# Performance work log

Hardware: AMD Instinct MI355X
Metric: run time of the kernel (lower is better)

The kernel has to match this reference:

```python
import math
import jax, jax.numpy as jnp
import numpy as np

H = 16          # num attention heads
D = 64          # head dim
BUCKETS = 256   # position_buckets
MAX_POS = 512   # max_relative_positions
ATT_SPAN = BUCKETS  # pos_ebd_size A
SCALE_FACTOR = 3    # 1 + len(['c2p','p2c'])


def _log_bucket(rel):
    # log-bucketed relative positions (DeBERTa-v2 _make_log_bucket_position)
    mid = BUCKETS // 2
    rel = jnp.clip(rel, -MAX_POS + 1, MAX_POS - 1)
    sign = jnp.sign(rel).astype(jnp.float32)
    abs_pos = jnp.maximum(jnp.abs(rel), 1)
    log_base = math.log((MAX_POS - 1) / mid)
    log_pos = jnp.ceil(jnp.log(abs_pos.astype(jnp.float32) / mid) / log_base * (mid - 1)) + mid
    bucket = jnp.where(abs_pos < mid, abs_pos.astype(jnp.float32), log_pos) * sign
    return bucket.astype(jnp.int32)


def _rel_pos(q_len, k_len):
    q = jnp.arange(q_len, dtype=jnp.int32)
    k = jnp.arange(k_len, dtype=jnp.int32)
    return _log_bucket(q[:, None] - k[None, :])  # (Q, K)


def setup_inputs() -> dict:
    key = jax.random.key(0)
    ks = jax.random.split(key, 6)
    B, S, Hd = 4, 1024, 1024
    std = 0.02
    return {
        "hidden_states": jax.random.normal(ks[0], (B, S, Hd), jnp.float32),
        "rel_embeddings": jax.random.normal(ks[1], (2 * ATT_SPAN, Hd), jnp.float32) * std,
        "Wq": jax.random.normal(ks[2], (Hd, H * D), jnp.float32) * std,
        "bq": jnp.zeros((H * D,), jnp.float32),
        "Wk": jax.random.normal(ks[3], (Hd, H * D), jnp.float32) * std,
        "bk": jnp.zeros((H * D,), jnp.float32),
        "Wv": jax.random.normal(ks[4], (Hd, H * D), jnp.float32) * std,
        "bv": jnp.zeros((H * D,), jnp.float32),
    }


def reference(hidden_states, rel_embeddings, Wq, bq, Wk, bk, Wv, bv):
    B, S, Hd = hidden_states.shape
    A2 = 2 * ATT_SPAN

    def heads(x):  # (B,S,H*D) -> (B,H,S,D)
        return x.reshape(B, S, H, D).transpose(0, 2, 1, 3)

    q = heads(hidden_states @ Wq + bq)
    k = heads(hidden_states @ Wk + bk)
    v = heads(hidden_states @ Wv + bv)

    scale = math.sqrt(D * SCALE_FACTOR)
    scores = jnp.einsum('bhqd,bhkd->bhqk', q, k) / scale  # (B,H,S,S)

    rel = _rel_pos(S, S)  # (S,S) int32 bucketed relative ids
    # share_att_key=True: pos key/query use key_proj/query_proj
    pos_k = (rel_embeddings @ Wk + bk).reshape(A2, H, D).transpose(1, 0, 2)  # (H,2A,D)
    pos_q = (rel_embeddings @ Wq + bq).reshape(A2, H, D).transpose(1, 0, 2)  # (H,2A,D)

    # c2p: content->position
    c2p = jnp.einsum('bhqd,hkd->bhqk', q, pos_k)  # (B,H,S,2A)
    c2p_idx = jnp.clip(rel + ATT_SPAN, 0, A2 - 1)  # (S,S)
    c2p = jnp.take_along_axis(c2p, jnp.broadcast_to(c2p_idx[None, None], (B, H, S, S)), axis=-1) / scale

    # p2c: position->content
    p2c = jnp.einsum('bhkd,hqd->bhkq', k, pos_q)  # (B,H,S,2A)
    p2c_idx = jnp.clip(-rel + ATT_SPAN, 0, A2 - 1)  # (S,S)
    p2c = jnp.take_along_axis(p2c, jnp.broadcast_to(p2c_idx[None, None], (B, H, S, S)), axis=-1)
    p2c = jnp.swapaxes(p2c, -1, -2) / scale

    probs = jax.nn.softmax(scores + c2p + p2c, axis=-1)
    ctx = jnp.einsum('bhqk,bhkd->bhqd', probs, v)  # (B,H,S,D)
    return ctx.transpose(0, 2, 1, 3).reshape(B, S, H * D)
```

## Files before the change

### kernel.cpp

```cpp
#include <hip/hip_runtime.h>
#include <hip/hip_bf16.h>
#include <math.h>

typedef __attribute__((ext_vector_type(8))) short v8s;
typedef __attribute__((ext_vector_type(4))) short v4sh;
typedef __attribute__((ext_vector_type(4))) unsigned short v4us;
typedef __attribute__((ext_vector_type(4))) float v4f;
typedef __attribute__((ext_vector_type(4))) int   v4i;

#define AS1(p) ((const __attribute__((address_space(1))) void*)(p))
#define AS3(p) ((__attribute__((address_space(3))) void*)(p))

__device__ inline unsigned short f2b(float f){
  __hip_bfloat16 h = __float2bfloat16(f);
  return __builtin_bit_cast(unsigned short, h);
}
__device__ inline float b2f(unsigned short u){
  __hip_bfloat16 h = __builtin_bit_cast(__hip_bfloat16, u);
  return __bfloat162float(h);
}
__device__ inline unsigned cvtpk(float lo, float hi){
  unsigned d;
  asm("v_cvt_pk_bf16_f32 %0, %1, %2" : "=v"(d) : "v"(lo), "v"(hi));
  return d;
}

__device__ inline int bucket_id(int i){
  int r = i - 1023;
  if (r > 511) r = 511; if (r < -511) r = -511;
  float sign = (r > 0) ? 1.f : ((r < 0) ? -1.f : 0.f);
  int ap = r < 0 ? -r : r; if (ap < 1) ap = 1;
  float bucket;
  if (ap < 128) bucket = (float)ap * sign;
  else {
    float lp = ceilf(logf((float)ap / 128.f) / logf(511.f/128.f) * 127.f) + 128.f;
    bucket = lp * sign;
  }
  int idx = (int)bucket + 256;
  if (idx < 0) idx = 0; if (idx > 511) idx = 511;
  return idx;
}

__global__ __launch_bounds__(256) void pack_x(const float* __restrict__ hs,
                                              const float* __restrict__ rel,
                                              const float* __restrict__ Wq,
                                              const float* __restrict__ Wk,
                                              const float* __restrict__ Wv,
                                              unsigned short* __restrict__ X,
                                              unsigned short* __restrict__ Wt3,
                                              short* __restrict__ tab,
                                              unsigned long long* __restrict__ tab64){
  __shared__ unsigned short t[64][65];
  int blk = blockIdx.x;
  if (blk < 2304){
    const int HT8 = 4096*1024/8;
    int i8 = blk*256 + threadIdx.x;
    const float* src = (i8 < HT8) ? (hs + (size_t)i8*8) : (rel + ((size_t)i8 - HT8)*8);
    v8s o;
    #pragma unroll
    for (int j = 0; j < 8; j++) o[j] = (short)f2b(src[j]);
    *(v8s*)&X[(size_t)i8*8] = o;
    return;
  }
  if (blk < 2313){
    int i = (blk - 2304)*256 + threadIdx.x;
    if (i < 2047) tab[i] = (short)bucket_id(i);
    if (i < 2056){
      unsigned long long w = 0;
      #pragma unroll
      for (int r = 0; r < 4; r++)
        w |= (unsigned long long)(unsigned short)bucket_id(i + r) << (16*r);
      tab64[i] = w;
    }
    return;
  }
  int tb = blk - 2313;
  int wsel = tb >> 8, bx = tb & 255;
  const float* in = (wsel == 0) ? Wq : ((wsel == 1) ? Wk : Wv);
  unsigned short* outp = Wt3 + ((size_t)wsel << 20);
  int r0 = (bx >> 4) << 6, c0 = (bx & 15) << 6;
  int tx = threadIdx.x & 63, ty = threadIdx.x >> 6;
  #pragma unroll
  for (int p = 0; p < 16; p++){ int r = (p<<2)+ty; t[tx][r] = f2b(in[(size_t)(r0+r)*1024 + c0+tx]); }
  __syncthreads();
  #pragma unroll
  for (int p = 0; p < 16; p++){ int c = (p<<2)+ty; outp[(size_t)(c0+c)*1024 + r0+tx] = t[c][tx]; }
}

__global__ __launch_bounds__(256) void gemm_qkv(
    const unsigned short* __restrict__ A,
    const unsigned short* __restrict__ Bt3,
    unsigned short* __restrict__ Qa, unsigned short* __restrict__ Ka,
    unsigned short* __restrict__ VtT,
    const float* __restrict__ bq, const float* __restrict__ bk,
    const float* __restrict__ bv, float alpha_q)
{
  __shared__ unsigned short smem[2*128*64];
  unsigned short* a_tile = smem;
  unsigned short* b_tile = smem + 128*64;
  int nb = (blockIdx.x & 7)*108 + (blockIdx.x >> 3);
  int bm = nb / 24, bn = nb % 24;
  int m0 = bm << 7, n0 = bn << 7;
  int tid = threadIdx.x, lane = tid & 63, wave = tid >> 6;
  int l15 = lane & 15, lhi = lane >> 4;
  int rbase = (wave >> 1) << 6, cbase = (wave & 1) << 6;
  int crow[4], csw[4];
  #pragma unroll
  for (int u = 0; u < 4; u++){
    int ch = tid + (u << 8);
    crow[u] = ch >> 3;
    csw[u] = ((ch & 7) ^ (crow[u] & 7)) << 3;
  }
  v4f acc[4][4] = {};
  for (int kt = 0; kt < 1024; kt += 64){
    #pragma unroll
    for (int u = 0; u < 4; u++){
      int ch = tid + (u << 8);
      __builtin_amdgcn_global_load_lds(AS1(A   + (size_t)(m0 + crow[u])*1024 + kt + csw[u]),
                                       AS3(a_tile + (size_t)ch*8), 16, 0, 0);
      __builtin_amdgcn_global_load_lds(AS1(Bt3 + (size_t)(n0 + crow[u])*1024 + kt + csw[u]),
                                       AS3(b_tile + (size_t)ch*8), 16, 0, 0);
    }
    __syncthreads();
    #pragma unroll
    for (int ks = 0; ks < 2; ks++){
      v8s af[4], bfr[4];
      int kb = (ks << 2) + lhi;
      #pragma unroll
      for (int i = 0; i < 4; i++){
        int r = rbase + (i << 4) + l15;
        af[i] = *(const v8s*)&a_tile[r*64 + ((kb ^ (r & 7)) << 3)];
      }
      #pragma unroll
      for (int j = 0; j < 4; j++){
        int r = cbase + (j << 4) + l15;
        bfr[j] = *(const v8s*)&b_tile[r*64 + ((kb ^ (r & 7)) << 3)];
      }
      #pragma unroll
      for (int i = 0; i < 4; i++)
        #pragma unroll
        for (int j = 0; j < 4; j++)
          acc[i][j] = __builtin_amdgcn_mfma_f32_16x16x32_bf16(af[i], bfr[j], acc[i][j], 0, 0, 0);
    }
    __syncthreads();
  }
  int seg = n0 >> 10;
  int nn0 = n0 & 1023;
  if (seg == 2){
    if (m0 >= 4096) return;
    int bb = m0 >> 10, s0 = m0 & 1023;
    #pragma unroll
    for (int i = 0; i < 4; i++){
      int r = rbase + (i << 4) + (lhi << 2);
      #pragma unroll
      for (int j = 0; j < 4; j++){
        int c = cbase + (j << 4) + l15;
        float bvv = bv[nn0 + c];
        #pragma unroll
        for (int rr = 0; rr < 4; rr++)
          smem[c*128 + ((r + rr) ^ ((c & 7) << 4))] = f2b(acc[i][j][rr] + bvv);
      }
    }
    __syncthreads();
    int v = tid >> 3, sc = (tid & 7) << 4;
    #pragma unroll
    for (int vb = 0; vb < 4; vb++){
      int vv = v + (vb << 5);
      #pragma unroll
      for (int c2 = 0; c2 < 2; c2++){
        int sb = sc + (c2 << 3);
        v8s val = *(const v8s*)&smem[vv*128 + (sb ^ ((vv & 7) << 4))];
        *(v8s*)&VtT[((size_t)(bb << 10) + nn0 + vv)*1024 + s0 + sb] = val;
      }
    }
    return;
  }
  unsigned short* C = (seg == 0) ? Qa : Ka;
  const float* bias = (seg == 0) ? bq : bk;
  float alpha = (seg == 0) ? alpha_q : 1.f;
  #pragma unroll
  for (int i = 0; i < 4; i++){
    int row = m0 + rbase + (i << 4) + (lhi << 2);
    #pragma unroll
    for (int j = 0; j < 4; j++){
      int col = nn0 + cbase + (j << 4) + l15;
      float bvv = bias[col];
      #pragma unroll
      for (int r = 0; r < 4; r++)
        C[(size_t)(row + r)*1024 + col] = f2b((acc[i][j][r] + bvv) * alpha);
    }
  }
}

__global__ __launch_bounds__(256) void gemm_pos(
    const unsigned short* __restrict__ Qa,
    const unsigned short* __restrict__ Ka,
    unsigned short* __restrict__ C2P,
    unsigned short* __restrict__ P2C)
{
  __shared__ unsigned short a_tile[128*64];
  __shared__ unsigned short b_tile[128*64];
  int tab = blockIdx.y >> 4, h = blockIdx.y & 15;
  int bm = blockIdx.x >> 2, bn = blockIdx.x & 3;
  int m0 = bm << 7, n0 = bn << 7;
  const unsigned short* A  = tab ? Ka : Qa;
  const unsigned short* Bt = tab ? Qa : Ka;
  unsigned short* C = tab ? P2C : C2P;
  int tid = threadIdx.x, lane = tid & 63, wave = tid >> 6;
  int l15 = lane & 15, lhi = lane >> 4;
  int rbase = (wave >> 1) << 6, cbase = (wave & 1) << 6;
  #pragma unroll
  for (int u = 0; u < 4; u++){
    int ch = tid + (u << 8);
    int row = ch >> 3;
    int csw = ((ch & 7) ^ (row & 7)) << 3;
    __builtin_amdgcn_global_load_lds(AS1(A  + (size_t)(m0 + row)*1024 + (h << 6) + csw),
                                     AS3(a_tile + (size_t)ch*8), 16, 0, 0);
    __builtin_amdgcn_global_load_lds(AS1(Bt + (size_t)(4096 + n0 + row)*1024 + (h << 6) + csw),
                                     AS3(b_tile + (size_t)ch*8), 16, 0, 0);
  }
  __syncthreads();
  v4f acc[4][4] = {};
  #pragma unroll
  for (int ks = 0; ks < 2; ks++){
    v8s af[4], bfr[4];
    int kb = (ks << 2) + lhi;
    #pragma unroll
    for (int i = 0; i < 4; i++){
      int r = rbase + (i << 4) + l15;
      af[i] = *(const v8s*)&a_tile[r*64 + ((kb ^ (r & 7)) << 3)];
    }
    #pragma unroll
    for (int j = 0; j < 4; j++){
      int r = cbase + (j << 4) + l15;
      bfr[j] = *(const v8s*)&b_tile[r*64 + ((kb ^ (r & 7)) << 3)];
    }
    #pragma unroll
    for (int i = 0; i < 4; i++)
      #pragma unroll
      for (int j = 0; j < 4; j++)
        acc[i][j] = __builtin_amdgcn_mfma_f32_16x16x32_bf16(af[i], bfr[j], acc[i][j], 0, 0, 0);
  }
  #pragma unroll
  for (int i = 0; i < 4; i++){
    int row = m0 + rbase + (i << 4) + (lhi << 2);
    #pragma unroll
    for (int j = 0; j < 4; j++){
      int col = n0 + cbase + (j << 4) + l15;
      #pragma unroll
      for (int r = 0; r < 4; r++)
        C[(size_t)(row + r)*8192 + (h << 9) + col] = f2b(acc[i][j][r]);
    }
  }
}

__global__ __launch_bounds__(256) void attn(
  const unsigned short* __restrict__ Qall,
  const unsigned short* __restrict__ Kall,
  const unsigned short* __restrict__ Vt,
  const unsigned short* __restrict__ c2p,
  const unsigned short* __restrict__ p2c,
  const short* __restrict__ idxt,
  const unsigned long long* __restrict__ t64g,
  float* __restrict__ out)
{
  __shared__ unsigned short k_lds[64*64];
  __shared__ unsigned short v_lds[2][64*64];
  __shared__ unsigned short cw[64*72];
  __shared__ unsigned short pw[64*72];
  __shared__ short basc[16*64];
  __shared__ short basp[16*64];

  int bid = blockIdx.x;
  int xcd = bid & 7, jj = bid >> 3;
  int bh = (xcd << 3) + (jj >> 4), qb = jj & 15;
  int b = bh >> 4, h = bh & 15;
  int q0 = qb << 6;
  int tid = threadIdx.x, lane = tid & 63, wave = tid >> 6;
  int l15 = lane & 15, lhi = lane >> 4;

  #pragma unroll
  for (int v = 0; v < 8; v++){
    int i = tid + (v << 8);
    int kt = (i >> 6) & 15, row = i & 63;
    if (i < 1024){
      int bc = idxt[q0 + row - (kt << 6) + 960] & ~7;
      basc[(kt << 6) + row] = (short)(row*72 - bc);
    } else {
      int bp = idxt[q0 + 1023 - (kt << 6) - row] & ~7;
      basp[(kt << 6) + row] = (short)(row*72 - bp);
    }
  }

  int qrow = q0 + (wave << 4) + l15;
  v8s aq[2];
  #pragma unroll
  for (int ks = 0; ks < 2; ks++)
    aq[ks] = *(const v8s*)&Qall[(size_t)((b << 10) + qrow)*1024 + (h << 6) + (ks << 5) + (lhi << 3)];

  int prow_[3], pcc_[3]; bool pval[3];
  #pragma unroll
  for (int u = 0; u < 3; u++){
    int pp = tid + (u << 8);
    pval[u] = pp < 576;
    prow_[u] = pp / 9; pcc_[u] = pp - prow_[u]*9;
  }
  const size_t cbase0 = ((size_t)((b << 10) + q0))*8192 + (h << 9);
  const size_t pbase0 = ((size_t)(b << 10))*8192 + (h << 9);

  unsigned long long t64u[4];

  auto issue_kwin = [&](int kt){
    int k0 = kt << 6;
    #pragma unroll
    for (int u = 0; u < 2; u++){
      int ch = tid + (u << 8);
      int rr = ch >> 3, seg = ch & 7;
      int csw = (seg ^ (rr & 7)) << 3;
      __builtin_amdgcn_global_load_lds(AS1(Kall + (size_t)((b << 10) + k0 + rr)*1024 + (h << 6) + csw),
                                       AS3(k_lds + (size_t)ch*8), 16, 0, 0);
    }
    #pragma unroll
    for (int u = 0; u < 3; u++){
      if (pval[u]){
        int row = prow_[u], cc = pcc_[u];
        int bc = row*72 - (int)basc[(kt << 6) + row];
        __builtin_amdgcn_global_load_lds(AS1(c2p + cbase0 + (size_t)row*8192 + bc + (cc << 3)),
                                         AS3(cw + (size_t)(tid + (u << 8))*8), 16, 0, 0);
        int bp = row*72 - (int)basp[(kt << 6) + row];
        __builtin_amdgcn_global_load_lds(AS1(p2c + pbase0 + (size_t)(k0 + row)*8192 + bp + (cc << 3)),
                                         AS3(pw + (size_t)(tid + (u << 8))*8), 16, 0, 0);
      }
    }
  };
  auto issue_tv = [&](int kt, int sel){
    int k0 = kt << 6;
    int Bc = q0 - k0 + (wave << 4) + l15 - (lhi << 2) + 1020;
    #pragma unroll
    for (int j = 0; j < 4; j++) t64u[j] = t64g[Bc - (j << 4)];
    __builtin_amdgcn_sched_barrier(0);
    #pragma unroll
    for (int u = 0; u < 2; u++){
      int ch = tid + (u << 8);
      int rr = ch >> 3, seg = ch & 7;
      int csw = (seg ^ (rr & 7)) << 3;
      __builtin_amdgcn_global_load_lds(AS1(Vt + (size_t)((b << 10) + (h << 6) + rr)*1024 + k0 + csw),
                                       AS3(&v_lds[sel][0] + (size_t)ch*8), 16, 0, 0);
    }
  };

  v4f o_acc[4] = {};
  float m_run = -INFINITY, l_part = 0.f;

  __syncthreads();
  issue_kwin(0);
  __builtin_amdgcn_sched_barrier(0);
  issue_tv(0, 0);

  for (int kt = 0; kt < 16; kt++){
    asm volatile("s_waitcnt vmcnt(6)" ::: "memory");
    __builtin_amdgcn_sched_barrier(0);
    __builtin_amdgcn_s_barrier();
    __builtin_amdgcn_sched_barrier(0);

    v4f s_acc[4] = {};
    #pragma unroll
    for (int j = 0; j < 4; j++){
      int krow = (j << 4) + l15;
      #pragma unroll
      for (int ks = 0; ks < 2; ks++){
        v8s kf = *(const v8s*)&k_lds[krow*64 + ((((ks << 2) + lhi) ^ (krow & 7)) << 3)];
        s_acc[j] = __builtin_amdgcn_mfma_f32_16x16x32_bf16(kf, aq[ks], s_acc[j], 0, 0, 0);
      }
    }
    int cvq = (int)basc[(kt << 6) + (wave << 4) + l15];
    #pragma unroll
    for (int j = 0; j < 4; j++){
      v4sh bp4 = *(const v4sh*)&basp[(kt << 6) + (j << 4) + (lhi << 2)];
      v4us idv = __builtin_bit_cast(v4us, t64u[j]);
      #pragma unroll
      for (int r = 0; r < 4; r++){
        int id = (int)idv[3 - r];
        s_acc[j][r] += b2f(cw[cvq + id]) + b2f(pw[(int)bp4[r] + id]);
      }
    }
    float lmax = s_acc[0][0];
    #pragma unroll
    for (int j = 0; j < 4; j++)
      #pragma unroll
      for (int r = 0; r < 4; r++) lmax = fmaxf(lmax, s_acc[j][r]);
    if (__any(lmax > m_run + 6.f)){
      float mx = lmax;
      mx = fmaxf(mx, __shfl_xor(mx, 16));
      mx = fmaxf(mx, __shfl_xor(mx, 32));
      float mnew = fmaxf(m_run, mx);
      float corr = exp2f(m_run - mnew);
      m_run = mnew;
      l_part *= corr;
      float co[4];
      #pragma unroll
      for (int r = 0; r < 4; r++) co[r] = __shfl(corr, (lhi << 2) + r);
      #pragma unroll
      for (int j = 0; j < 4; j++)
        #pragma unroll
        for (int r = 0; r < 4; r++) o_acc[j][r] *= co[r];
    }
    unsigned wj[4][2];
    float ps = 0.f;
    #pragma unroll
    for (int j = 0; j < 4; j++){
      float p0 = exp2f(s_acc[j][0] - m_run);
      float p1 = exp2f(s_acc[j][1] - m_run);
      float p2 = exp2f(s_acc[j][2] - m_run);
      float p3 = exp2f(s_acc[j][3] - m_run);
      ps += (p0 + p1) + (p2 + p3);
      wj[j][0] = cvtpk(p0, p1);
      wj[j][1] = cvtpk(p2, p3);
    }
    l_part += ps;
    #pragma unroll
    for (int p = 0; p < 2; p++){
      asm("v_permlane32_swap_b32 %0, %1" : "+v"(wj[0][p]), "+v"(wj[1][p]));
      asm("v_permlane32_swap_b32 %0, %1" : "+v"(wj[2][p]), "+v"(wj[3][p]));
      asm("v_permlane16_swap_b32 %0, %1" : "+v"(wj[0][p]), "+v"(wj[1][p]));
      asm("v_permlane16_swap_b32 %0, %1" : "+v"(wj[2][p]), "+v"(wj[3][p]));
    }
    v4i pai0 = { (int)wj[0][0], (int)wj[0][1], (int)wj[1][0], (int)wj[1][1] };
    v4i pai1 = { (int)wj[2][0], (int)wj[2][1], (int)wj[3][0], (int)wj[3][1] };
    v8s pa0 = __builtin_bit_cast(v8s, pai0);
    v8s pa1 = __builtin_bit_cast(v8s, pai1);

    asm volatile("s_waitcnt vmcnt(0)" ::: "memory");
    __builtin_amdgcn_sched_barrier(0);
    __builtin_amdgcn_s_barrier();
    __builtin_amdgcn_sched_barrier(0);

    if (kt < 15) issue_kwin(kt + 1);
    __builtin_amdgcn_sched_barrier(0);

    const unsigned short* vl = &v_lds[kt & 1][0];
    #pragma unroll
    for (int j = 0; j < 4; j++){
      int vrow = (j << 4) + l15;
      v8s vb0 = *(const v8s*)&vl[vrow*64 + (((lhi) ^ (vrow & 7)) << 3)];
      o_acc[j] = __builtin_amdgcn_mfma_f32_16x16x32_bf16(pa0, vb0, o_acc[j], 0, 0, 0);
      v8s vb1 = *(const v8s*)&vl[vrow*64 + (((4 + lhi) ^ (vrow & 7)) << 3)];
      o_acc[j] = __builtin_amdgcn_mfma_f32_16x16x32_bf16(pa1, vb1, o_acc[j], 0, 0, 0);
    }
    __builtin_amdgcn_sched_barrier(0);
    if (kt < 15) issue_tv(kt + 1, (kt + 1) & 1);
  }
  float ls = l_part;
  ls += __shfl_xor(ls, 16);
  ls += __shfl_xor(ls, 32);
  float inv = 1.f / ls;
  float io[4];
  #pragma unroll
  for (int r = 0; r < 4; r++) io[r] = __shfl(inv, (lhi << 2) + r);
  #pragma unroll
  for (int r = 0; r < 4; r++){
    int row = q0 + (wave << 4) + (lhi << 2) + r;
    #pragma unroll
    for (int j = 0; j < 4; j++)
      out[(size_t)((b << 10) + row)*1024 + (h << 6) + (j << 4) + l15] = o_acc[j][r] * io[r];
  }
}

extern "C" void kernel_launch(void* const* d_in, const int* in_sizes, int n_in,
                              void* d_out, int out_size, void* d_ws, size_t ws_size,
                              hipStream_t stream)
{
  const float* hs  = (const float*)d_in[0];
  const float* rel = (const float*)d_in[1];
  const float* Wq  = (const float*)d_in[2];
  const float* bq  = (const float*)d_in[3];
  const float* Wk  = (const float*)d_in[4];
  const float* bk  = (const float*)d_in[5];
  const float* Wv  = (const float*)d_in[6];
  const float* bv  = (const float*)d_in[7];
  float* out = (float*)d_out;

  char* ws = (char*)d_ws;
  size_t off = 0;
  auto alloc = [&](size_t bytes) -> void* {
    void* p = ws + off; off += (bytes + 255) & ~(size_t)255; return p;
  };
  short*              idxt  = (short*)             alloc(2047 * 2);
  unsigned long long* tab64 = (unsigned long long*)alloc(2056 * 8);
  unsigned short* Xb   = (unsigned short*)alloc((size_t)4608*1024*2);
  unsigned short* Wt3  = (unsigned short*)alloc((size_t)3072*1024*2);
  unsigned short* Qa   = (unsigned short*)alloc((size_t)4608*1024*2);
  unsigned short* Ka   = (unsigned short*)alloc((size_t)4608*1024*2);
  unsigned short* VtT  = (unsigned short*)alloc((size_t)4096*1024*2);
  unsigned short* C2P  = (unsigned short*)alloc((size_t)4096*8192*2);
  unsigned short* P2C  = (unsigned short*)alloc((size_t)4096*8192*2);
  (void)                                  alloc(4096);
  (void)ws_size; (void)in_sizes; (void)n_in; (void)out_size;

  pack_x<<<3081, 256, 0, stream>>>(hs, rel, Wq, Wk, Wv, Xb, Wt3, idxt, tab64);

  const float alpha_q = 1.4426950408889634f / sqrtf(192.f);
  gemm_qkv<<<864, 256, 0, stream>>>(Xb, Wt3, Qa, Ka, VtT, bq, bk, bv, alpha_q);

  gemm_pos<<<dim3(128, 32), 256, 0, stream>>>(Qa, Ka, C2P, P2C);

  attn<<<1024, 256, 0, stream>>>(Qa, Ka, VtT, C2P, P2C, idxt, tab64, out);
}
```

Baseline: 167.6 us.

## Stage GEMM epilogues through LDS for coalesced stores; single-buffer V tile

The projection and positional GEMM epilogues now write bf16 results into a swizzled LDS tile, then store them with coalesced 16-byte vector writes instead of scattered 2-byte global stores. In the attention kernel the double-buffered V tile becomes a single buffer, with an extra barrier before the next V prefetch. This cuts LDS use, which may raise occupancy, at the cost of an added sync per iteration and less overlap between the PV matmul and the next V load.

```diff
diff --git a/kernel.cpp b/kernel.cpp
--- a/kernel.cpp
+++ b/kernel.cpp
@@ -180,15 +180,23 @@
   float alpha = (seg == 0) ? alpha_q : 1.f;
   #pragma unroll
   for (int i = 0; i < 4; i++){
-    int row = m0 + rbase + (i << 4) + (lhi << 2);
-    #pragma unroll
-    for (int j = 0; j < 4; j++){
-      int col = nn0 + cbase + (j << 4) + l15;
-      float bvv = bias[col];
+    int row = rbase + (i << 4) + (lhi << 2);
+    #pragma unroll
+    for (int j = 0; j < 4; j++){
+      int col = cbase + (j << 4) + l15;
+      float bvv = bias[nn0 + col];
       #pragma unroll
       for (int r = 0; r < 4; r++)
-        C[(size_t)(row + r)*1024 + col] = f2b((acc[i][j][r] + bvv) * alpha);
-    }
+        smem[(row + r)*128 + (col ^ (((row + r) & 7) << 4))] = f2b((acc[i][j][r] + bvv) * alpha);
+    }
+  }
+  __syncthreads();
+  #pragma unroll
+  for (int c = 0; c < 8; c++){
+    int row = (tid >> 4) + (c << 4);
+    int col8 = (tid & 15) << 3;
+    v8s val = *(const v8s*)&smem[row*128 + (col8 ^ ((row & 7) << 4))];
+    *(v8s*)&C[(size_t)(m0 + row)*1024 + nn0 + col8] = val;
   }
 }
 
@@ -198,8 +206,9 @@
     unsigned short* __restrict__ C2P,
     unsigned short* __restrict__ P2C)
 {
-  __shared__ unsigned short a_tile[128*64];
-  __shared__ unsigned short b_tile[128*64];
+  __shared__ unsigned short smem[2*128*64];
+  unsigned short* a_tile = smem;
+  unsigned short* b_tile = smem + 128*64;
   int tab = blockIdx.y >> 4, h = blockIdx.y & 15;
   int bm = blockIdx.x >> 2, bn = blockIdx.x & 3;
   int m0 = bm << 7, n0 = bn << 7;
@@ -241,16 +250,25 @@
       for (int j = 0; j < 4; j++)
         acc[i][j] = __builtin_amdgcn_mfma_f32_16x16x32_bf16(af[i], bfr[j], acc[i][j], 0, 0, 0);
   }
+  __syncthreads();
   #pragma unroll
   for (int i = 0; i < 4; i++){
-    int row = m0 + rbase + (i << 4) + (lhi << 2);
-    #pragma unroll
-    for (int j = 0; j < 4; j++){
-      int col = n0 + cbase + (j << 4) + l15;
+    int row = rbase + (i << 4) + (lhi << 2);
+    #pragma unroll
+    for (int j = 0; j < 4; j++){
+      int col = cbase + (j << 4) + l15;
       #pragma unroll
       for (int r = 0; r < 4; r++)
-        C[(size_t)(row + r)*8192 + (h << 9) + col] = f2b(acc[i][j][r]);
-    }
+        smem[(row + r)*128 + (col ^ (((row + r) & 7) << 4))] = f2b(acc[i][j][r]);
+    }
+  }
+  __syncthreads();
+  #pragma unroll
+  for (int c = 0; c < 8; c++){
+    int row = (tid >> 4) + (c << 4);
+    int col8 = (tid & 15) << 3;
+    v8s val = *(const v8s*)&smem[row*128 + (col8 ^ ((row & 7) << 4))];
+    *(v8s*)&C[(size_t)(m0 + row)*8192 + (h << 9) + n0 + col8] = val;
   }
 }
 
@@ -265,7 +283,7 @@
   float* __restrict__ out)
 {
   __shared__ unsigned short k_lds[64*64];
-  __shared__ unsigned short v_lds[2][64*64];
+  __shared__ unsigned short v_lds[64*64];
   __shared__ unsigned short cw[64*72];
   __shared__ unsigned short pw[64*72];
   __shared__ short basc[16*64];
@@ -327,13 +345,13 @@
         int bc = row*72 - (int)basc[(kt << 6) + row];
         __builtin_amdgcn_global_load_lds(AS1(c2p + cbase0 + (size_t)row*8192 + bc + (cc << 3)),
                                          AS3(cw + (size_t)(tid + (u << 8))*8), 16, 0, 0);
-        int bp = row*72 - (int)basp[(kt << 6) + row];
+      int bp = row*72 - (int)basp[(kt << 6) + row];
         __builtin_amdgcn_global_load_lds(AS1(p2c + pbase0 + (size_t)(k0 + row)*8192 + bp + (cc << 3)),
                                          AS3(pw + (size_t)(tid + (u << 8))*8), 16, 0, 0);
       }
     }
   };
-  auto issue_tv = [&](int kt, int sel){
+  auto issue_tv = [&](int kt){
     int k0 = kt << 6;
     int Bc = q0 - k0 + (wave << 4) + l15 - (lhi << 2) + 1020;
     #pragma unroll
@@ -345,7 +363,7 @@
       int rr = ch >> 3, seg = ch & 7;
       int csw = (seg ^ (rr & 7)) << 3;
       __builtin_amdgcn_global_load_lds(AS1(Vt + (size_t)((b << 10) + (h << 6) + rr)*1024 + k0 + csw),
-                                       AS3(&v_lds[sel][0] + (size_t)ch*8), 16, 0, 0);
+                                       AS3(v_lds + (size_t)ch*8), 16, 0, 0);
     }
   };
 
@@ -355,7 +373,7 @@
   __syncthreads();
   issue_kwin(0);
   __builtin_amdgcn_sched_barrier(0);
-  issue_tv(0, 0);
+  issue_tv(0);
 
   for (int kt = 0; kt < 16; kt++){
     asm volatile("s_waitcnt vmcnt(6)" ::: "memory");
@@ -438,17 +456,21 @@
     if (kt < 15) issue_kwin(kt + 1);
     __builtin_amdgcn_sched_barrier(0);
 
-    const unsigned short* vl = &v_lds[kt & 1][0];
     #pragma unroll
     for (int j = 0; j < 4; j++){
       int vrow = (j << 4) + l15;
-      v8s vb0 = *(const v8s*)&vl[vrow*64 + (((lhi) ^ (vrow & 7)) << 3)];
+      v8s vb0 = *(const v8s*)&v_lds[vrow*64 + (((lhi) ^ (vrow & 7)) << 3)];
       o_acc[j] = __builtin_amdgcn_mfma_f32_16x16x32_bf16(pa0, vb0, o_acc[j], 0, 0, 0);
-      v8s vb1 = *(const v8s*)&vl[vrow*64 + (((4 + lhi) ^ (vrow & 7)) << 3)];
+      v8s vb1 = *(const v8s*)&v_lds[vrow*64 + (((4 + lhi) ^ (vrow & 7)) << 3)];
       o_acc[j] = __builtin_amdgcn_mfma_f32_16x16x32_bf16(pa1, vb1, o_acc[j], 0, 0, 0);
     }
-    __builtin_amdgcn_sched_barrier(0);
-    if (kt < 15) issue_tv(kt + 1, (kt + 1) & 1);
+    if (kt < 15){
+      asm volatile("s_waitcnt lgkmcnt(0)" ::: "memory");
+      __builtin_amdgcn_sched_barrier(0);
+      __builtin_amdgcn_s_barrier();
+      __builtin_amdgcn_sched_barrier(0);
+      issue_tv(kt + 1);
+    }
   }
   float ls = l_part;
   ls += __shfl_xor(ls, 16);
```

After: 158.5 us. 5.4% less time.
